# Optimization experiments

Measured on AMD Instinct MI355X. Metric: run time of the kernel, lower is better.

Reference implementation:

```python
import jax, jax.numpy as jnp
import numpy as np

B, N, H, F_IN, F_OUT = 16, 512, 8, 128, 128
NEG_SLOPE = 0.2


def setup_inputs() -> dict:
    key = jax.random.key(0)
    k_h, k_adj, k_bias, k_W, k_a = jax.random.split(key, 5)
    h = jax.random.normal(k_h, (B, N, F_IN), dtype=jnp.float32)
    # Binary adjacency (shared across batch); force self-loops so every row
    # of the masked softmax has at least one valid entry (avoids NaN rows).
    adj = jax.random.randint(k_adj, (N, N), 0, 2, dtype=jnp.int32)
    adj = adj.at[jnp.arange(N), jnp.arange(N)].set(1)
    bias_matrix = jax.random.normal(k_bias, (1, 1, N, N), dtype=jnp.float32)
    # Xavier-uniform-like init for params
    lim_W = float(np.sqrt(6.0 / (F_IN + F_OUT)))
    W = jax.random.uniform(k_W, (H, F_IN, F_OUT), minval=-lim_W, maxval=lim_W, dtype=jnp.float32)
    lim_a = float(np.sqrt(6.0 / (2 * F_OUT + 1)))
    a = jax.random.uniform(k_a, (H, 2 * F_OUT, 1), minval=-lim_a, maxval=lim_a, dtype=jnp.float32)
    return {"h": h, "adj": adj, "bias_matrix": bias_matrix, "W": W, "a": a}


def reference(h, adj, bias_matrix, W, a):
    # h: [B,N,Fin], adj: [N,N] int, bias_matrix: [1,1,N,N], W: [H,Fin,F], a: [H,2F,1]
    f = W.shape[-1]
    h_prime = jnp.einsum('bni,hio->bnho', h, W)  # [B,N,H,F]
    # e[b,i,j,h] = leakyrelu(a_h . concat(h_prime[b,i,h], h_prime[b,j,h]))
    # Decompose a into src/dst halves: identical math, avoids O(B*N*N*H*2F) cat.
    a_src = a[:, :f, 0]  # [H,F]
    a_dst = a[:, f:, 0]  # [H,F]
    s_src = jnp.einsum('bnhf,hf->bnh', h_prime, a_src)  # score contribution of node i
    s_dst = jnp.einsum('bnhf,hf->bnh', h_prime, a_dst)  # score contribution of node j
    e = jax.nn.leaky_relu(s_src[:, :, None, :] + s_dst[:, None, :, :], NEG_SLOPE)  # [B,N,N,H]
    e = e + bias_matrix[0, 0][None, :, :, None]  # bias broadcast over batch & heads
    mask = (adj != 0)[None, :, :, None]  # [1,N,N,1] -> broadcast [B,N,N,H]
    e = jnp.where(mask, e, -jnp.inf)
    attention = jax.nn.softmax(e, axis=2)  # softmax over neighbors j
    h_out = jnp.einsum('bijh,bjhf->bihf', attention, h_prime)  # [B,N,H,F]
    # concat=False -> mean over heads
    return h_out.mean(axis=2)  # [B,N,F]
```

## Files before the change

### kernel.cpp

```cpp
#include <hip/hip_runtime.h>
#include <hip/hip_bf16.h>

#define NB 16
#define NN 512
#define NH 8
#define NF 128
#define NEG_SLOPE 0.2f

typedef short bf16x8 __attribute__((ext_vector_type(8)));
typedef unsigned short u16x8 __attribute__((ext_vector_type(8)));
typedef float f32x4 __attribute__((ext_vector_type(4)));

__device__ inline unsigned short f2bf(float x) {
    __hip_bfloat16 b = __float2bfloat16(x);
    return __builtin_bit_cast(unsigned short, b);
}
__device__ inline float bf2f(unsigned short u) {
    return __uint_as_float(((unsigned int)u) << 16);
}

__global__ __launch_bounds__(256) void prep_all_kernel(
    const float* __restrict__ h, const int* __restrict__ adj,
    const float* __restrict__ bias, const float* __restrict__ W,
    const float* __restrict__ a,
    unsigned short* __restrict__ emb,
    unsigned short* __restrict__ hHi, unsigned short* __restrict__ hLo,
    unsigned short* __restrict__ wtHi, unsigned short* __restrict__ wtLo,
    float* __restrict__ wasrc, float* __restrict__ wadst)
{
    int t = blockIdx.x * 256 + threadIdx.x;
    {
        float v = h[t];
        unsigned short hi = f2bf(v);
        hHi[t] = hi;
        hLo[t] = f2bf(v - bf2f(hi));
    }
    if (t < NN * NN) emb[t] = (adj[t] != 0) ? f2bf(__expf(bias[t])) : (unsigned short)0;
    if (t < NH * NF * NF) {
        float v = W[t];
        int hh = t >> 14;
        int k  = (t >> 7) & 127;
        int f  = t & 127;
        int u  = (hh * NF + f) * NF + k;
        unsigned short hi = f2bf(v);
        wtHi[u] = hi;
        wtLo[u] = f2bf(v - bf2f(hi));
    }
    if (t < NH * NF) {
        int hh = t >> 7, i = t & 127;
        const float4* wrow = (const float4*)(W + (hh * NF + i) * NF);
        const float4* asr = (const float4*)(a + hh * 2 * NF);
        const float4* ads = (const float4*)(a + hh * 2 * NF + NF);
        float s1 = 0.f, s2 = 0.f;
        #pragma unroll 8
        for (int f = 0; f < NF / 4; ++f) {
            float4 w = wrow[f], x = asr[f], y = ads[f];
            s1 += w.x * x.x + w.y * x.y + w.z * x.z + w.w * x.w;
            s2 += w.x * y.x + w.y * y.y + w.z * y.z + w.w * y.w;
        }
        wasrc[t] = s1; wadst[t] = s2;
    }
}

__global__ __launch_bounds__(256) void score_kernel(
    const float* __restrict__ h, const float* __restrict__ wasrc,
    const float* __restrict__ wadst, float* __restrict__ ssrc, float* __restrict__ sdstT)
{
    __shared__ float wsm[2][NH * (NF + 4)];
    int tid = threadIdx.x;
    for (int u = tid; u < NH * NF; u += 256) {
        int hh = u >> 7, f = u & 127;
        wsm[0][hh * (NF + 4) + f] = wasrc[u];
        wsm[1][hh * (NF + 4) + f] = wadst[u];
    }
    __syncthreads();
    int t = blockIdx.x * 256 + tid;
    int hh = t & 7;
    int bn = t >> 3;
    int b = bn >> 9, n = bn & 511;
    const float4* hrow = (const float4*)(h + (size_t)bn * NF);
    const float4* w1 = (const float4*)(&wsm[0][hh * (NF + 4)]);
    const float4* w2 = (const float4*)(&wsm[1][hh * (NF + 4)]);
    float s1 = 0.f, s2 = 0.f;
    #pragma unroll
    for (int u = 0; u < NF / 4; ++u) {
        float4 hv = hrow[u], a1 = w1[u], a2 = w2[u];
        s1 += hv.x * a1.x + hv.y * a1.y + hv.z * a1.z + hv.w * a1.w;
        s2 += hv.x * a2.x + hv.y * a2.y + hv.z * a2.z + hv.w * a2.w;
    }
    ssrc[t] = s1;
    sdstT[((size_t)(b * NH + hh)) * NN + n] = s2;
}

__global__ __launch_bounds__(256, 4) void hprime_kernel(
    const unsigned short* __restrict__ hHi, const unsigned short* __restrict__ hLo,
    const unsigned short* __restrict__ wtHi, const unsigned short* __restrict__ wtLo,
    unsigned short* __restrict__ hpT)
{
    int bx = blockIdx.x;
    int nchunk = bx & 63;
    int hfg = bx >> 6;
    int hh = hfg >> 1, fg = hfg & 1;
    int tid = threadIdx.x;
    int wave = tid >> 6, lane = tid & 63;
    int col = lane & 15, kg = lane >> 4;
    int fbase = hh * NF + fg * 64 + wave * 16;
    int n0g = nchunk * 128;
    int b = n0g >> 9;
    int nin = n0g & 511;

    const unsigned short* Bh = wtHi + (size_t)(fbase + col) * NF + kg * 8;
    const unsigned short* Bl = wtLo + (size_t)(fbase + col) * NF + kg * 8;
    bf16x8 bh[4], bl[4];
    #pragma unroll
    for (int ks = 0; ks < 4; ++ks) {
        bh[ks] = *(const bf16x8*)(Bh + ks * 32);
        bl[ks] = *(const bf16x8*)(Bl + ks * 32);
    }

    size_t outRow = ((size_t)b * (NH * NF) + fbase + col) * NN;

    #pragma unroll 2
    for (int nt = 0; nt < 8; ++nt) {
        const unsigned short* Ah = hHi + (size_t)(n0g + nt * 16 + col) * NF + kg * 8;
        const unsigned short* Al = hLo + (size_t)(n0g + nt * 16 + col) * NF + kg * 8;
        bf16x8 ah[4], al[4];
        #pragma unroll
        for (int ks = 0; ks < 4; ++ks) {
            ah[ks] = *(const bf16x8*)(Ah + ks * 32);
            al[ks] = *(const bf16x8*)(Al + ks * 32);
        }
        f32x4 acc = {0.f, 0.f, 0.f, 0.f};
        #pragma unroll
        for (int ks = 0; ks < 4; ++ks) {
            acc = __builtin_amdgcn_mfma_f32_16x16x32_bf16(ah[ks], bh[ks], acc, 0, 0, 0);
            acc = __builtin_amdgcn_mfma_f32_16x16x32_bf16(al[ks], bh[ks], acc, 0, 0, 0);
            acc = __builtin_amdgcn_mfma_f32_16x16x32_bf16(ah[ks], bl[ks], acc, 0, 0, 0);
        }
        ushort4 u;
        u.x = f2bf(acc[0]); u.y = f2bf(acc[1]);
        u.z = f2bf(acc[2]); u.w = f2bf(acc[3]);
        *(ushort4*)&hpT[outRow + nin + nt * 16 + kg * 4] = u;
    }
}

__device__ inline bf16x8 make_afrag(float s, float4 v0, float4 v1, bf16x8 eb) {
    u16x8 ebu = __builtin_bit_cast(u16x8, eb);
    u16x8 r;
    float x;
    x = s + v0.x; x = fmaxf(x, NEG_SLOPE * x); r[0] = f2bf(__expf(x) * bf2f(ebu[0]));
    x = s + v0.y; x = fmaxf(x, NEG_SLOPE * x); r[1] = f2bf(__expf(x) * bf2f(ebu[1]));
    x = s + v0.z; x = fmaxf(x, NEG_SLOPE * x); r[2] = f2bf(__expf(x) * bf2f(ebu[2]));
    x = s + v0.w; x = fmaxf(x, NEG_SLOPE * x); r[3] = f2bf(__expf(x) * bf2f(ebu[3]));
    x = s + v1.x; x = fmaxf(x, NEG_SLOPE * x); r[4] = f2bf(__expf(x) * bf2f(ebu[4]));
    x = s + v1.y; x = fmaxf(x, NEG_SLOPE * x); r[5] = f2bf(__expf(x) * bf2f(ebu[5]));
    x = s + v1.z; x = fmaxf(x, NEG_SLOPE * x); r[6] = f2bf(__expf(x) * bf2f(ebu[6]));
    x = s + v1.w; x = fmaxf(x, NEG_SLOPE * x); r[7] = f2bf(__expf(x) * bf2f(ebu[7]));
    return __builtin_bit_cast(bf16x8, r);
}

__global__ __launch_bounds__(512, 2) void attn_kernel(
    const unsigned short* __restrict__ hpT, const unsigned short* __restrict__ emb,
    const float* __restrict__ ssrc, const float* __restrict__ sdstT,
    float* __restrict__ out)
{
    __shared__ float red[NH][16][NF + 4];
    int bx = blockIdx.x;
    int b = bx & 15;
    int ipair = bx >> 4;
    int i0 = ipair * 32;
    int tid = threadIdx.x;
    int lane = tid & 63, h = tid >> 6;
    int col = lane & 15, kg = lane >> 4;

    const short one_bf = (short)0x3f80;
    const bf16x8 vone = {one_bf, one_bf, one_bf, one_bf, one_bf, one_bf, one_bf, one_bf};

    const float* sd = sdstT + (size_t)(b * NH + h) * NN;
    float s0 = ssrc[((size_t)(b * NN) + i0 + col) * NH + h];
    float s1 = ssrc[((size_t)(b * NN) + i0 + 16 + col) * NH + h];
    const unsigned short* eb0p = emb + (size_t)(i0 + col) * NN;
    const unsigned short* eb1p = emb + (size_t)(i0 + 16 + col) * NN;
    const unsigned short* Bbase = hpT + ((size_t)(b * NH + h) * NF + col) * NN;

    f32x4 acc[2][8];
    f32x4 accS[2];
    #pragma unroll
    for (int ti = 0; ti < 2; ++ti) {
        accS[ti] = (f32x4){0.f, 0.f, 0.f, 0.f};
        #pragma unroll
        for (int tf = 0; tf < 8; ++tf) acc[ti][tf] = (f32x4){0.f, 0.f, 0.f, 0.f};
    }

    float4 sv0[2], sv1[2];
    bf16x8 eb0v[2], eb1v[2];
    {
        int j = kg * 8;
        sv0[0] = *(const float4*)(sd + j);
        sv1[0] = *(const float4*)(sd + j + 4);
        eb0v[0] = *(const bf16x8*)(eb0p + j);
        eb1v[0] = *(const bf16x8*)(eb1p + j);
    }

    #pragma unroll
    for (int t = 0; t < 16; ++t) {
        const int cur = t & 1, nxt = cur ^ 1;
        const int jc = t * 32 + kg * 8;
        if (t < 15) {
            const int jn = jc + 32;
            sv0[nxt] = *(const float4*)(sd + jn);
            sv1[nxt] = *(const float4*)(sd + jn + 4);
            eb0v[nxt] = *(const bf16x8*)(eb0p + jn);
            eb1v[nxt] = *(const bf16x8*)(eb1p + jn);
        }
        bf16x8 Bv[8];
        #pragma unroll
        for (int tf = 0; tf < 8; ++tf)
            Bv[tf] = *(const bf16x8*)(Bbase + (size_t)tf * 16 * NN + jc);

        bf16x8 A0 = make_afrag(s0, sv0[cur], sv1[cur], eb0v[cur]);
        bf16x8 A1 = make_afrag(s1, sv0[cur], sv1[cur], eb1v[cur]);

        __builtin_amdgcn_s_setprio(1);
        #pragma unroll
        for (int tf = 0; tf < 8; ++tf) {
            acc[0][tf] = __builtin_amdgcn_mfma_f32_16x16x32_bf16(A0, Bv[tf], acc[0][tf], 0, 0, 0);
            acc[1][tf] = __builtin_amdgcn_mfma_f32_16x16x32_bf16(A1, Bv[tf], acc[1][tf], 0, 0, 0);
        }
        accS[0] = __builtin_amdgcn_mfma_f32_16x16x32_bf16(A0, vone, accS[0], 0, 0, 0);
        accS[1] = __builtin_amdgcn_mfma_f32_16x16x32_bf16(A1, vone, accS[1], 0, 0, 0);
        __builtin_amdgcn_s_setprio(0);
    }

    int fr = tid & 127;
    int iq = tid >> 7;
    #pragma unroll
    for (int ti = 0; ti < 2; ++ti) {
        #pragma unroll
        for (int tf = 0; tf < 8; ++tf)
            #pragma unroll
            for (int r = 0; r < 4; ++r)
                red[h][kg * 4 + r][tf * 16 + col] = acc[ti][tf][r] / accS[ti][r];
        __syncthreads();
        #pragma unroll
        for (int q = 0; q < 4; ++q) {
            int i = iq * 4 + q;
            float sacc = 0.f;
            #pragma unroll
            for (int w = 0; w < NH; ++w) sacc += red[w][i][fr];
            out[((size_t)(b * NN) + i0 + ti * 16 + i) * NF + fr] = sacc * 0.125f;
        }
        if (ti == 0) __syncthreads();
    }
}

extern "C" void kernel_launch(void* const* d_in, const int* in_sizes, int n_in,
                              void* d_out, int out_size, void* d_ws, size_t ws_size,
                              hipStream_t stream)
{
    const float* h    = (const float*)d_in[0];
    const int*   adj  = (const int*)d_in[1];
    const float* bias = (const float*)d_in[2];
    const float* W    = (const float*)d_in[3];
    const float* a    = (const float*)d_in[4];
    float* out = (float*)d_out;

    char* ws = (char*)d_ws;
    unsigned short* hpT  = (unsigned short*)ws;   ws += (size_t)NB * NH * NF * NN * 2;
    unsigned short* emb  = (unsigned short*)ws;   ws += (size_t)NN * NN * 2;
    float* ssrc  = (float*)ws;                    ws += (size_t)NB * NN * NH * 4;
    float* sdstT = (float*)ws;                    ws += (size_t)NB * NN * NH * 4;
    float* wasrc = (float*)ws;                    ws += NH * NF * 4;
    float* wadst = (float*)ws;                    ws += NH * NF * 4;
    unsigned short* hHi  = (unsigned short*)ws;   ws += (size_t)NB * NN * NF * 2;
    unsigned short* hLo  = (unsigned short*)ws;   ws += (size_t)NB * NN * NF * 2;
    unsigned short* wtHi = (unsigned short*)ws;   ws += (size_t)NH * NF * NF * 2;
    unsigned short* wtLo = (unsigned short*)ws;   ws += (size_t)NH * NF * NF * 2;

    hipLaunchKernelGGL(prep_all_kernel, dim3((NB * NN * NF) / 256), dim3(256), 0, stream,
                       h, adj, bias, W, a, emb, hHi, hLo, wtHi, wtLo, wasrc, wadst);
    hipLaunchKernelGGL(score_kernel, dim3((NB * NN * NH) / 256), dim3(256), 0, stream,
                       h, wasrc, wadst, ssrc, sdstT);
    hipLaunchKernelGGL(hprime_kernel, dim3(64 * 16), dim3(256), 0, stream,
                       hHi, hLo, wtHi, wtLo, hpT);
    hipLaunchKernelGGL(attn_kernel, dim3(NB * 16), dim3(512), 0, stream,
                       hpT, emb, ssrc, sdstT, out);
}
```

Baseline: 161.2 us.

## Reassociate attention to aggregate raw features before per-head projection

Instead of materialising per-head projected features h' and aggregating them, the attention kernel now aggregates the raw bf16 input features (shared across heads) and then multiplies the aggregated result by W per head with MFMA. This removes the hprime kernel and its large per-head intermediate buffer, cutting memory traffic since the aggregation operand is one tensor shared by all heads rather than one per head. The prep kernel now writes a transposed bf16 copy of h via LDS. The attention grid doubles to 16-row tiles with higher occupancy. The risks are extra precision loss from rounding the aggregated features to bf16 before the projection, and an added per-block projection GEMM.

After: 173.4 us. 7.6% more time.

```diff
diff --git a/kernel.cpp b/kernel.cpp
--- a/kernel.cpp
+++ b/kernel.cpp
@@ -19,34 +19,58 @@
     return __uint_as_float(((unsigned int)u) << 16);
 }
 
-__global__ __launch_bounds__(256) void prep_all_kernel(
+__global__ __launch_bounds__(256) void prep_kernel(
     const float* __restrict__ h, const int* __restrict__ adj,
     const float* __restrict__ bias, const float* __restrict__ W,
     const float* __restrict__ a,
-    unsigned short* __restrict__ emb,
-    unsigned short* __restrict__ hHi, unsigned short* __restrict__ hLo,
+    unsigned short* __restrict__ emb, unsigned short* __restrict__ hT,
     unsigned short* __restrict__ wtHi, unsigned short* __restrict__ wtLo,
     float* __restrict__ wasrc, float* __restrict__ wadst)
 {
-    int t = blockIdx.x * 256 + threadIdx.x;
-    {
-        float v = h[t];
-        unsigned short hi = f2bf(v);
-        hHi[t] = hi;
-        hLo[t] = f2bf(v - bf2f(hi));
-    }
-    if (t < NN * NN) emb[t] = (adj[t] != 0) ? f2bf(__expf(bias[t])) : (unsigned short)0;
-    if (t < NH * NF * NF) {
-        float v = W[t];
-        int hh = t >> 14;
-        int k  = (t >> 7) & 127;
-        int f  = t & 127;
-        int u  = (hh * NF + f) * NF + k;
-        unsigned short hi = f2bf(v);
-        wtHi[u] = hi;
-        wtLo[u] = f2bf(v - bf2f(hi));
-    }
-    if (t < NH * NF) {
+    __shared__ unsigned short lds[2][128][136];
+    int bx = blockIdx.x, tid = threadIdx.x;
+    if (bx < 1024) {
+        int t = bx * 256 + tid;
+        emb[t] = (adj[t] != 0) ? f2bf(__expf(bias[t])) : (unsigned short)0;
+    } else if (bx < 1088) {
+        int bi = bx - 1024;
+        int b = bi >> 2, nq = bi & 3;
+        #pragma unroll 4
+        for (int e = 0; e < 64; ++e) {
+            int idx = e * 256 + tid;
+            int nl = idx >> 7, f = idx & 127;
+            float v = h[((size_t)(b * NN) + nq * 128 + nl) * NF + f];
+            lds[0][f][nl] = f2bf(v);
+        }
+        __syncthreads();
+        int k = tid >> 1, nh2 = tid & 1;
+        #pragma unroll
+        for (int u = 0; u < 8; ++u) {
+            *(u16x8*)&hT[((size_t)(b * NF) + k) * NN + nq * 128 + nh2 * 64 + u * 8] =
+                *(const u16x8*)&lds[0][k][nh2 * 64 + u * 8];
+        }
+    } else if (bx < 1096) {
+        int h8 = bx - 1088;
+        #pragma unroll 4
+        for (int e = 0; e < 64; ++e) {
+            int idx = e * 256 + tid;
+            int k = idx >> 7, f = idx & 127;
+            float v = W[((size_t)(h8 * NF) + k) * NF + f];
+            unsigned short hi = f2bf(v);
+            lds[0][f][k] = hi;
+            lds[1][f][k] = f2bf(v - bf2f(hi));
+        }
+        __syncthreads();
+        int f = tid >> 1, kh = tid & 1;
+        #pragma unroll
+        for (int u = 0; u < 8; ++u) {
+            int off = kh * 64 + u * 8;
+            size_t go = ((size_t)(h8 * NF) + f) * NF + off;
+            *(u16x8*)&wtHi[go] = *(const u16x8*)&lds[0][f][off];
+            *(u16x8*)&wtLo[go] = *(const u16x8*)&lds[1][f][off];
+        }
+    } else {
+        int t = (bx - 1096) * 256 + tid;
         int hh = t >> 7, i = t & 127;
         const float4* wrow = (const float4*)(W + (hh * NF + i) * NF);
         const float4* asr = (const float4*)(a + hh * 2 * NF);
@@ -90,58 +114,6 @@
     }
     ssrc[t] = s1;
     sdstT[((size_t)(b * NH + hh)) * NN + n] = s2;
-}
-
-__global__ __launch_bounds__(256, 4) void hprime_kernel(
-    const unsigned short* __restrict__ hHi, const unsigned short* __restrict__ hLo,
-    const unsigned short* __restrict__ wtHi, const unsigned short* __restrict__ wtLo,
-    unsigned short* __restrict__ hpT)
-{
-    int bx = blockIdx.x;
-    int nchunk = bx & 63;
-    int hfg = bx >> 6;
-    int hh = hfg >> 1, fg = hfg & 1;
-    int tid = threadIdx.x;
-    int wave = tid >> 6, lane = tid & 63;
-    int col = lane & 15, kg = lane >> 4;
-    int fbase = hh * NF + fg * 64 + wave * 16;
-    int n0g = nchunk * 128;
-    int b = n0g >> 9;
-    int nin = n0g & 511;
-
-    const unsigned short* Bh = wtHi + (size_t)(fbase + col) * NF + kg * 8;
-    const unsigned short* Bl = wtLo + (size_t)(fbase + col) * NF + kg * 8;
-    bf16x8 bh[4], bl[4];
-    #pragma unroll
-    for (int ks = 0; ks < 4; ++ks) {
-        bh[ks] = *(const bf16x8*)(Bh + ks * 32);
-        bl[ks] = *(const bf16x8*)(Bl + ks * 32);
-    }
-
-    size_t outRow = ((size_t)b * (NH * NF) + fbase + col) * NN;
-
-    #pragma unroll 2
-    for (int nt = 0; nt < 8; ++nt) {
-        const unsigned short* Ah = hHi + (size_t)(n0g + nt * 16 + col) * NF + kg * 8;
-        const unsigned short* Al = hLo + (size_t)(n0g + nt * 16 + col) * NF + kg * 8;
-        bf16x8 ah[4], al[4];
-        #pragma unroll
-        for (int ks = 0; ks < 4; ++ks) {
-            ah[ks] = *(const bf16x8*)(Ah + ks * 32);
-            al[ks] = *(const bf16x8*)(Al + ks * 32);
-        }
-        f32x4 acc = {0.f, 0.f, 0.f, 0.f};
-        #pragma unroll
-        for (int ks = 0; ks < 4; ++ks) {
-            acc = __builtin_amdgcn_mfma_f32_16x16x32_bf16(ah[ks], bh[ks], acc, 0, 0, 0);
-            acc = __builtin_amdgcn_mfma_f32_16x16x32_bf16(al[ks], bh[ks], acc, 0, 0, 0);
-            acc = __builtin_amdgcn_mfma_f32_16x16x32_bf16(ah[ks], bl[ks], acc, 0, 0, 0);
-        }
-        ushort4 u;
-        u.x = f2bf(acc[0]); u.y = f2bf(acc[1]);
-        u.z = f2bf(acc[2]); u.w = f2bf(acc[3]);
-        *(ushort4*)&hpT[outRow + nin + nt * 16 + kg * 4] = u;
-    }
 }
 
 __device__ inline bf16x8 make_afrag(float s, float4 v0, float4 v1, bf16x8 eb) {
@@ -159,99 +131,128 @@
     return __builtin_bit_cast(bf16x8, r);
 }
 
-__global__ __launch_bounds__(512, 2) void attn_kernel(
-    const unsigned short* __restrict__ hpT, const unsigned short* __restrict__ emb,
+__global__ __launch_bounds__(512, 4) void attn_kernel(
+    const unsigned short* __restrict__ hT, const unsigned short* __restrict__ emb,
     const float* __restrict__ ssrc, const float* __restrict__ sdstT,
+    const unsigned short* __restrict__ wtHi, const unsigned short* __restrict__ wtLo,
     float* __restrict__ out)
 {
-    __shared__ float red[NH][16][NF + 4];
+    __shared__ float red[NH][16][136];
     int bx = blockIdx.x;
     int b = bx & 15;
-    int ipair = bx >> 4;
-    int i0 = ipair * 32;
+    int it = bx >> 4;
+    int i0 = it * 16;
     int tid = threadIdx.x;
-    int lane = tid & 63, h = tid >> 6;
+    int lane = tid & 63, hh = tid >> 6;
     int col = lane & 15, kg = lane >> 4;
 
     const short one_bf = (short)0x3f80;
     const bf16x8 vone = {one_bf, one_bf, one_bf, one_bf, one_bf, one_bf, one_bf, one_bf};
 
-    const float* sd = sdstT + (size_t)(b * NH + h) * NN;
-    float s0 = ssrc[((size_t)(b * NN) + i0 + col) * NH + h];
-    float s1 = ssrc[((size_t)(b * NN) + i0 + 16 + col) * NH + h];
-    const unsigned short* eb0p = emb + (size_t)(i0 + col) * NN;
-    const unsigned short* eb1p = emb + (size_t)(i0 + 16 + col) * NN;
-    const unsigned short* Bbase = hpT + ((size_t)(b * NH + h) * NF + col) * NN;
-
-    f32x4 acc[2][8];
-    f32x4 accS[2];
-    #pragma unroll
-    for (int ti = 0; ti < 2; ++ti) {
-        accS[ti] = (f32x4){0.f, 0.f, 0.f, 0.f};
-        #pragma unroll
-        for (int tf = 0; tf < 8; ++tf) acc[ti][tf] = (f32x4){0.f, 0.f, 0.f, 0.f};
-    }
-
-    float4 sv0[2], sv1[2];
-    bf16x8 eb0v[2], eb1v[2];
-    {
-        int j = kg * 8;
-        sv0[0] = *(const float4*)(sd + j);
-        sv1[0] = *(const float4*)(sd + j + 4);
-        eb0v[0] = *(const bf16x8*)(eb0p + j);
-        eb1v[0] = *(const bf16x8*)(eb1p + j);
-    }
-
+    const float* sd = sdstT + (size_t)(b * NH + hh) * NN;
+    float s0 = ssrc[((size_t)(b * NN) + i0 + col) * NH + hh];
+    const unsigned short* ebp = emb + (size_t)(i0 + col) * NN;
+    const unsigned short* Bb = hT + ((size_t)(b * NF) + col) * NN;
+
+    f32x4 acc[8];
+    f32x4 accS = {0.f, 0.f, 0.f, 0.f};
+    #pragma unroll
+    for (int q = 0; q < 8; ++q) acc[q] = (f32x4){0.f, 0.f, 0.f, 0.f};
+
+    float4 svA0 = *(const float4*)(sd + kg * 8);
+    float4 svA1 = *(const float4*)(sd + kg * 8 + 4);
+    bf16x8 ebA = *(const bf16x8*)(ebp + kg * 8);
+    bf16x8 Ba[4];
+    #pragma unroll
+    for (int q = 0; q < 4; ++q)
+        Ba[q] = *(const bf16x8*)(Bb + (size_t)(q * 16) * NN + kg * 8);
+
+    float4 svB0, svB1; bf16x8 ebB;
     #pragma unroll
     for (int t = 0; t < 16; ++t) {
-        const int cur = t & 1, nxt = cur ^ 1;
-        const int jc = t * 32 + kg * 8;
+        int jc = t * 32 + kg * 8;
+        bf16x8 Bhi[4];
+        #pragma unroll
+        for (int q = 0; q < 4; ++q)
+            Bhi[q] = *(const bf16x8*)(Bb + (size_t)((4 + q) * 16) * NN + jc);
         if (t < 15) {
-            const int jn = jc + 32;
-            sv0[nxt] = *(const float4*)(sd + jn);
-            sv1[nxt] = *(const float4*)(sd + jn + 4);
-            eb0v[nxt] = *(const bf16x8*)(eb0p + jn);
-            eb1v[nxt] = *(const bf16x8*)(eb1p + jn);
-        }
-        bf16x8 Bv[8];
-        #pragma unroll
-        for (int tf = 0; tf < 8; ++tf)
-            Bv[tf] = *(const bf16x8*)(Bbase + (size_t)tf * 16 * NN + jc);
-
-        bf16x8 A0 = make_afrag(s0, sv0[cur], sv1[cur], eb0v[cur]);
-        bf16x8 A1 = make_afrag(s1, sv0[cur], sv1[cur], eb1v[cur]);
-
+            svB0 = *(const float4*)(sd + jc + 32);
+            svB1 = *(const float4*)(sd + jc + 36);
+            ebB  = *(const bf16x8*)(ebp + jc + 32);
+        }
+        bf16x8 A = make_afrag(s0, svA0, svA1, ebA);
         __builtin_amdgcn_s_setprio(1);
-        #pragma unroll
-        for (int tf = 0; tf < 8; ++tf) {
-            acc[0][tf] = __builtin_amdgcn_mfma_f32_16x16x32_bf16(A0, Bv[tf], acc[0][tf], 0, 0, 0);
-            acc[1][tf] = __builtin_amdgcn_mfma_f32_16x16x32_bf16(A1, Bv[tf], acc[1][tf], 0, 0, 0);
-        }
-        accS[0] = __builtin_amdgcn_mfma_f32_16x16x32_bf16(A0, vone, accS[0], 0, 0, 0);
-        accS[1] = __builtin_amdgcn_mfma_f32_16x16x32_bf16(A1, vone, accS[1], 0, 0, 0);
+        accS = __builtin_amdgcn_mfma_f32_16x16x32_bf16(A, vone, accS, 0, 0, 0);
+        #pragma unroll
+        for (int q = 0; q < 4; ++q)
+            acc[q] = __builtin_amdgcn_mfma_f32_16x16x32_bf16(A, Ba[q], acc[q], 0, 0, 0);
         __builtin_amdgcn_s_setprio(0);
-    }
-
-    int fr = tid & 127;
-    int iq = tid >> 7;
-    #pragma unroll
-    for (int ti = 0; ti < 2; ++ti) {
-        #pragma unroll
-        for (int tf = 0; tf < 8; ++tf)
+        if (t < 15) {
             #pragma unroll
-            for (int r = 0; r < 4; ++r)
-                red[h][kg * 4 + r][tf * 16 + col] = acc[ti][tf][r] / accS[ti][r];
-        __syncthreads();
-        #pragma unroll
-        for (int q = 0; q < 4; ++q) {
-            int i = iq * 4 + q;
-            float sacc = 0.f;
-            #pragma unroll
-            for (int w = 0; w < NH; ++w) sacc += red[w][i][fr];
-            out[((size_t)(b * NN) + i0 + ti * 16 + i) * NF + fr] = sacc * 0.125f;
-        }
-        if (ti == 0) __syncthreads();
-    }
+            for (int q = 0; q < 4; ++q)
+                Ba[q] = *(const bf16x8*)(Bb + (size_t)(q * 16) * NN + jc + 32);
+        }
+        __builtin_amdgcn_s_setprio(1);
+        #pragma unroll
+        for (int q = 0; q < 4; ++q)
+            acc[4 + q] = __builtin_amdgcn_mfma_f32_16x16x32_bf16(A, Bhi[q], acc[4 + q], 0, 0, 0);
+        __builtin_amdgcn_s_setprio(0);
+        if (t < 15) { svA0 = svB0; svA1 = svB1; ebA = ebB; }
+    }
+
+    f32x4 rinv;
+    #pragma unroll
+    for (int r = 0; r < 4; ++r) rinv[r] = 1.0f / accS[r];
+    #pragma unroll
+    for (int tk = 0; tk < 8; ++tk)
+        #pragma unroll
+        for (int r = 0; r < 4; ++r)
+            red[hh][kg * 4 + r][tk * 16 + col] = acc[tk][r] * rinv[r];
+
+    bf16x8 af[4];
+    #pragma unroll
+    for (int ks = 0; ks < 4; ++ks) {
+        float4 g0 = *(const float4*)&red[hh][col][ks * 32 + kg * 8];
+        float4 g1 = *(const float4*)&red[hh][col][ks * 32 + kg * 8 + 4];
+        u16x8 tmp;
+        tmp[0] = f2bf(g0.x); tmp[1] = f2bf(g0.y); tmp[2] = f2bf(g0.z); tmp[3] = f2bf(g0.w);
+        tmp[4] = f2bf(g1.x); tmp[5] = f2bf(g1.y); tmp[6] = f2bf(g1.z); tmp[7] = f2bf(g1.w);
+        af[ks] = __builtin_bit_cast(bf16x8, tmp);
+    }
+
+    f32x4 acc2[8];
+    #pragma unroll
+    for (int q = 0; q < 8; ++q) acc2[q] = (f32x4){0.f, 0.f, 0.f, 0.f};
+    const unsigned short* wh = wtHi + ((size_t)(hh * NF) + col) * NF + kg * 8;
+    const unsigned short* wl = wtLo + ((size_t)(hh * NF) + col) * NF + kg * 8;
+    #pragma unroll
+    for (int ft = 0; ft < 8; ++ft) {
+        #pragma unroll
+        for (int ks = 0; ks < 4; ++ks) {
+            bf16x8 bhv = *(const bf16x8*)(wh + (size_t)(ft * 16) * NF + ks * 32);
+            bf16x8 blv = *(const bf16x8*)(wl + (size_t)(ft * 16) * NF + ks * 32);
+            acc2[ft] = __builtin_amdgcn_mfma_f32_16x16x32_bf16(af[ks], bhv, acc2[ft], 0, 0, 0);
+            acc2[ft] = __builtin_amdgcn_mfma_f32_16x16x32_bf16(af[ks], blv, acc2[ft], 0, 0, 0);
+        }
+    }
+
+    #pragma unroll
+    for (int ft = 0; ft < 8; ++ft)
+        #pragma unroll
+        for (int r = 0; r < 4; ++r)
+            red[hh][kg * 4 + r][ft * 16 + col] = acc2[ft][r];
+    __syncthreads();
+
+    int i = tid >> 5;
+    int fq = (tid & 31) * 4;
+    float4 s = {0.f, 0.f, 0.f, 0.f};
+    #pragma unroll
+    for (int w = 0; w < NH; ++w) {
+        float4 v = *(const float4*)&red[w][i][fq];
+        s.x += v.x; s.y += v.y; s.z += v.z; s.w += v.w;
+    }
+    s.x *= 0.125f; s.y *= 0.125f; s.z *= 0.125f; s.w *= 0.125f;
+    *(float4*)&out[((size_t)(b * NN) + i0 + i) * NF + fq] = s;
 }
 
 extern "C" void kernel_launch(void* const* d_in, const int* in_sizes, int n_in,
@@ -266,23 +267,19 @@
     float* out = (float*)d_out;
 
     char* ws = (char*)d_ws;
-    unsigned short* hpT  = (unsigned short*)ws;   ws += (size_t)NB * NH * NF * NN * 2;
+    unsigned short* hT   = (unsigned short*)ws;   ws += (size_t)NB * NF * NN * 2;
     unsigned short* emb  = (unsigned short*)ws;   ws += (size_t)NN * NN * 2;
+    unsigned short* wtHi = (unsigned short*)ws;   ws += (size_t)NH * NF * NF * 2;
+    unsigned short* wtLo = (unsigned short*)ws;   ws += (size_t)NH * NF * NF * 2;
     float* ssrc  = (float*)ws;                    ws += (size_t)NB * NN * NH * 4;
     float* sdstT = (float*)ws;                    ws += (size_t)NB * NN * NH * 4;
     float* wasrc = (float*)ws;                    ws += NH * NF * 4;
     float* wadst = (float*)ws;                    ws += NH * NF * 4;
-    unsigned short* hHi  = (unsigned short*)ws;   ws += (size_t)NB * NN * NF * 2;
-    unsigned short* hLo  = (unsigned short*)ws;   ws += (size_t)NB * NN * NF * 2;
-    unsigned short* wtHi = (unsigned short*)ws;   ws += (size_t)NH * NF * NF * 2;
-    unsigned short* wtLo = (unsigned short*)ws;   ws += (size_t)NH * NF * NF * 2;
-
-    hipLaunchKernelGGL(prep_all_kernel, dim3((NB * NN * NF) / 256), dim3(256), 0, stream,
-                       h, adj, bias, W, a, emb, hHi, hLo, wtHi, wtLo, wasrc, wadst);
+
+    hipLaunchKernelGGL(prep_kernel, dim3(1100), dim3(256), 0, stream,
+                       h, adj, bias, W, a, emb, hT, wtHi, wtLo, wasrc, wadst);
     hipLaunchKernelGGL(score_kernel, dim3((NB * NN * NH) / 256), dim3(256), 0, stream,
                        h, wasrc, wadst, ssrc, sdstT);
-    hipLaunchKernelGGL(hprime_kernel, dim3(64 * 16), dim3(256), 0, stream,
-                       hHi, hLo, wtHi, wtLo, hpT);
-    hipLaunchKernelGGL(attn_kernel, dim3(NB * 16), dim3(512), 0, stream,
-                       hpT, emb, ssrc, sdstT, out);
-}
+    hipLaunchKernelGGL(attn_kernel, dim3(NB * 32), dim3(512), 0, stream,
+                       hT, emb, ssrc, sdstT, wtHi, wtLo, out);
+}
```
